# Kernel optimization log

Measured on AMD Instinct MI355X. Metric: run time of the kernel, lower is better.

## Reference

```python
import jax, jax.numpy as jnp
import numpy as np

B, N, IN_DIM, HEADS, PER_HEAD = 8, 512, 256, 4, 32
OUT_DIM = HEADS * PER_HEAD  # 128
NEG_SLOPE = 0.2


def setup_inputs() -> dict:
    key = jax.random.key(0)
    ks = jax.random.split(key, 8)
    x = jax.random.normal(ks[0], (B, N, IN_DIM), jnp.float32)
    adj = jax.random.randint(ks[1], (B, N, N), 0, 2, jnp.int32)
    sl = 1.0 / np.sqrt(IN_DIM)
    W_l = jax.random.normal(ks[2], (IN_DIM, OUT_DIM), jnp.float32) * sl  # source proj
    b_l = jnp.zeros((OUT_DIM,), jnp.float32)
    W_r = jax.random.normal(ks[3], (IN_DIM, OUT_DIM), jnp.float32) * sl  # target proj
    b_r = jnp.zeros((OUT_DIM,), jnp.float32)
    att = jax.random.normal(ks[4], (HEADS, PER_HEAD), jnp.float32) * (1.0 / np.sqrt(PER_HEAD))
    bias = jnp.zeros((OUT_DIM,), jnp.float32)
    return {"x": x, "adj": adj, "W_l": W_l, "b_l": b_l, "W_r": W_r, "b_r": b_r,
            "att": att, "bias": bias}


def _gatv2_single(x_b, adj_b, W_l, b_l, W_r, b_r, att, bias):
    # PyG GATv2Conv: remove_self_loops + add_self_loops -> diagonal forced to 1
    n = x_b.shape[0]
    adj_sl = jnp.fill_diagonal(adj_b, 1, inplace=False)
    # edge_index = adj.nonzero().t(): source = row, target = col
    m = (adj_sl != 0).T  # m[i, j]: source j feeds target i
    xl = (x_b @ W_l + b_l).reshape(n, HEADS, PER_HEAD)  # source-side features
    xr = (x_b @ W_r + b_r).reshape(n, HEADS, PER_HEAD)  # target-side features
    s = xr[:, None] + xl[None, :]                       # [i, j, H, C]
    s = jnp.where(s > 0, s, NEG_SLOPE * s)              # LeakyReLU(0.2)
    e = jnp.einsum('ijhc,hc->ijh', s, att)              # attention logits
    e = jnp.where(m[..., None], e, -jnp.inf)
    alpha = jax.nn.softmax(e, axis=1)                   # softmax over sources j
    out = jnp.einsum('ijh,jhc->ihc', alpha, xl).reshape(n, HEADS * PER_HEAD)
    return out + bias


def reference(x, adj, W_l, b_l, W_r, b_r, att, bias):
    # Sequential per-batch processing, faithful to the original Python loop
    # and keeping the [N,N,H,C] intermediate to one graph at a time.
    def one(args):
        x_b, adj_b = args
        return _gatv2_single(x_b, adj_b, W_l, b_l, W_r, b_r, att, bias)
    return jax.lax.map(one, (x, adj))  # [B, N, OUT_DIM]
```

## Files before the change

### kernel.cpp

```cpp
#include <hip/hip_runtime.h>
#include <hip/hip_bf16.h>

#define B_   8
#define N_   512
#define IND  256
#define H_   4
#define PH   32
#define OD   128
#define TI   4

typedef float v2f __attribute__((ext_vector_type(2)));

#define ATT_SCALE 0.5770780163555854f
#define DLR_SCALE 0.8656170245333781f

template <int PAT>
__device__ __forceinline__ float dpp_add(float x) {
    int yi = __builtin_amdgcn_mov_dpp(__float_as_int(x), PAT, 0xF, 0xF, true);
    return x + __int_as_float(yi);
}

__device__ __forceinline__ float fast_exp2(float x) {
#if __has_builtin(__builtin_amdgcn_exp2f)
    return __builtin_amdgcn_exp2f(x);
#else
    return exp2f(x);
#endif
}

__device__ __forceinline__ void pk_fma(v2f& d, v2f a, v2f b) {
    asm("v_pk_fma_f32 %0, %1, %2, %0" : "+v"(d) : "v"(a), "v"(b));
}

__global__ __launch_bounds__(256, 2) void proj_kernel(
    const float* __restrict__ x,
    const float* __restrict__ Wl, const float* __restrict__ bl,
    const float* __restrict__ Wr, const float* __restrict__ br,
    const float* __restrict__ att,
    float* __restrict__ xl, float* __restrict__ xr,
    float* __restrict__ dl, float* __restrict__ dr)
{
    __shared__ float xs[8 * IND];
    const int t = threadIdx.x;
    const int row0 = blockIdx.x * 8;

    const float4* xp4 = (const float4*)(x + (size_t)row0 * IND);
    float4* xs4 = (float4*)xs;
    #pragma unroll
    for (int k = 0; k < 2; ++k)
        xs4[t + k * 256] = xp4[t + k * 256];
    __syncthreads();

    const int which = t >> 7;
    const int rg = (t >> 6) & 1;
    const int og = t & 63;
    const int o0 = og * 2;
    const int r0 = rg * 4;
    const float* W  = which ? Wr : Wl;
    const float* bb = which ? br : bl;

    float acc0[4], acc1[4];
    #pragma unroll
    for (int r = 0; r < 4; ++r) { acc0[r] = 0.f; acc1[r] = 0.f; }

    for (int k = 0; k < IND; k += 4) {
        float wf0[4], wf1[4];
        #pragma unroll
        for (int kk = 0; kk < 4; ++kk) {
            float2 wv = *(const float2*)(W + (size_t)(k + kk) * OD + o0);
            wf0[kk] = wv.x;
            wf1[kk] = wv.y;
        }
        float xv[4][4];
        #pragma unroll
        for (int r = 0; r < 4; ++r)
            *(float4*)(xv[r]) = *(const float4*)(&xs[(r0 + r) * IND + k]);
        #pragma unroll
        for (int kk = 0; kk < 4; ++kk)
            #pragma unroll
            for (int r = 0; r < 4; ++r) {
                acc0[r] = fmaf(xv[r][kk], wf0[kk], acc0[r]);
                acc1[r] = fmaf(xv[r][kk], wf1[kk], acc1[r]);
            }
    }

    const float bv0 = bb[o0];
    const float bv1 = bb[o0 + 1];
    const float a0 = att[o0];
    const float a1 = att[o0 + 1];
    float* dst = which ? xr : xl;
    float* dp  = which ? dr : dl;
    float dcon[4];
    #pragma unroll
    for (int r = 0; r < 4; ++r) {
        float y0 = acc0[r] + bv0;
        float y1 = acc1[r] + bv1;
        *(float2*)(&dst[(size_t)(row0 + r0 + r) * OD + o0]) = make_float2(y0, y1);
        dcon[r] = fmaf(a0, y0, a1 * y1);
    }
    #pragma unroll
    for (int m = 1; m < 16; m <<= 1) {
        #pragma unroll
        for (int r = 0; r < 4; ++r)
            dcon[r] += __shfl_xor(dcon[r], m);
    }
    if ((og & 15) == 0) {
        const int h = og >> 4;
        #pragma unroll
        for (int r = 0; r < 4; ++r)
            dp[(size_t)(row0 + r0 + r) * H_ + h] = DLR_SCALE * dcon[r];
    }
}

__global__ __launch_bounds__(256, 3) void attn_kernel(
    const int* __restrict__ adj, const float* __restrict__ att,
    const float* __restrict__ bias,
    const float* __restrict__ xl, const float* __restrict__ xr,
    const float* __restrict__ dl, const float* __restrict__ dr,
    float* __restrict__ out)
{
    __shared__ float sacc[H_][16][TI][PH];
    __shared__ float ssum[H_][16][TI];

    const int t = threadIdx.x;
    const int b  = blockIdx.x >> 7;
    const int i0 = (blockIdx.x & 127) * TI;
    const int cq = t & 3;
    const int js = (t >> 2) & 15;
    const int h  = t >> 6;
    const int cbase = h * PH + cq * 8;

    float atS[8];
    {
        const float* ap = att + cbase;
        float4 a0 = *(const float4*)(ap);
        float4 a1 = *(const float4*)(ap + 4);
        atS[0] = ATT_SCALE * a0.x; atS[1] = ATT_SCALE * a0.y;
        atS[2] = ATT_SCALE * a0.z; atS[3] = ATT_SCALE * a0.w;
        atS[4] = ATT_SCALE * a1.x; atS[5] = ATT_SCALE * a1.y;
        atS[6] = ATT_SCALE * a1.z; atS[7] = ATT_SCALE * a1.w;
    }
    float xrS[TI][8];
    float drv[TI];
    #pragma unroll
    for (int il = 0; il < TI; ++il) {
        const float* xp = xr + ((size_t)(b * N_ + i0 + il)) * OD + cbase;
        float4 r0 = *(const float4*)(xp);
        float4 r1 = *(const float4*)(xp + 4);
        xrS[il][0] = r0.x; xrS[il][1] = r0.y; xrS[il][2] = r0.z; xrS[il][3] = r0.w;
        xrS[il][4] = r1.x; xrS[il][5] = r1.y; xrS[il][6] = r1.z; xrS[il][7] = r1.w;
        drv[il] = dr[((size_t)(b * N_ + i0 + il)) * H_ + h];
    }

    v2f acc[TI][4];
    float sumw[TI];
    #pragma unroll
    for (int il = 0; il < TI; ++il) {
        sumw[il] = 0.f;
        #pragma unroll
        for (int m = 0; m < 4; ++m) acc[il][m] = (v2f){0.f, 0.f};
    }

    const float* xlp = xl + ((size_t)(b * N_ + js)) * OD + cbase;
    const int*   ajp = adj + ((size_t)(b * N_ + js)) * N_ + i0;
    const float* dlp = dl + ((size_t)(b * N_ + js)) * H_ + h;

    float4 va = *(const float4*)(xlp);
    float4 vb = *(const float4*)(xlp + 4);
    int4   mj = *(const int4*)(ajp);
    float  dj = *dlp;

    #pragma unroll 2
    for (int u = 0; u < 32; ++u) {
        float4 wa = va, wb = vb;
        int4   wm = mj;
        float  wd = dj;
        if (u < 31) {
            xlp += 16 * OD; ajp += 16 * N_; dlp += 16 * H_;
            va = *(const float4*)(xlp);
            vb = *(const float4*)(xlp + 4);
            mj = *(const int4*)(ajp);
            dj = *dlp;
        }
        const int j = u * 16 + js;
        v2f p0 = (v2f){wa.x, wa.y}, p1 = (v2f){wa.z, wa.w};
        v2f p2 = (v2f){wb.x, wb.y}, p3 = (v2f){wb.z, wb.w};
        int wmv[4] = {wm.x, wm.y, wm.z, wm.w};
        #pragma unroll
        for (int il = 0; il < TI; ++il) {
            float s, e2a = 0.f, e2b = 0.f;
            s = xrS[il][0] + wa.x; e2a = fmaf(atS[0], __builtin_fabsf(s), e2a);
            s = xrS[il][1] + wa.y; e2b = fmaf(atS[1], __builtin_fabsf(s), e2b);
            s = xrS[il][2] + wa.z; e2a = fmaf(atS[2], __builtin_fabsf(s), e2a);
            s = xrS[il][3] + wa.w; e2b = fmaf(atS[3], __builtin_fabsf(s), e2b);
            s = xrS[il][4] + wb.x; e2a = fmaf(atS[4], __builtin_fabsf(s), e2a);
            s = xrS[il][5] + wb.y; e2b = fmaf(atS[5], __builtin_fabsf(s), e2b);
            s = xrS[il][6] + wb.z; e2a = fmaf(atS[6], __builtin_fabsf(s), e2a);
            s = xrS[il][7] + wb.w; e2b = fmaf(atS[7], __builtin_fabsf(s), e2b);
            float eh = e2a + e2b;
            eh = dpp_add<0xB1>(eh);
            eh = dpp_add<0x4E>(eh);
            float e = (wd + drv[il]) + eh;
            bool keep = (wmv[il] != 0) || (j == i0 + il);
            float w = keep ? fast_exp2(e) : 0.f;
            sumw[il] += w;
            v2f ws = (v2f){w, w};
            pk_fma(acc[il][0], ws, p0);
            pk_fma(acc[il][1], ws, p1);
            pk_fma(acc[il][2], ws, p2);
            pk_fma(acc[il][3], ws, p3);
        }
    }

    #pragma unroll
    for (int il = 0; il < TI; ++il) {
        float4 w0 = make_float4(acc[il][0].x, acc[il][0].y,
                                acc[il][1].x, acc[il][1].y);
        float4 w1 = make_float4(acc[il][2].x, acc[il][2].y,
                                acc[il][3].x, acc[il][3].y);
        *(float4*)(&sacc[h][js][il][cq * 8])     = w0;
        *(float4*)(&sacc[h][js][il][cq * 8 + 4]) = w1;
    }
    if (cq == 0) {
        #pragma unroll
        for (int il = 0; il < TI; ++il)
            ssum[h][js][il] = sumw[il];
    }
    __syncthreads();

    const int lane = t & 63;
    const int o = lane * 2;
    const int il2 = o >> 5;
    const int c2 = o & 31;
    float st = 0.f;
    #pragma unroll
    for (int k = 0; k < 16; ++k) st += ssum[h][k][il2];
    float a0 = 0.f, a1 = 0.f;
    #pragma unroll
    for (int k = 0; k < 16; ++k) {
        float2 p = *(const float2*)(&sacc[h][k][il2][c2]);
        a0 += p.x; a1 += p.y;
    }
    const float inv = 1.f / st;
    const int c = h * PH + c2;
    float* op = out + ((size_t)(b * N_ + i0 + il2)) * OD;
    *(float2*)(&op[c]) = make_float2(fmaf(a0, inv, bias[c]),
                                     fmaf(a1, inv, bias[c + 1]));
}

extern "C" void kernel_launch(void* const* d_in, const int* in_sizes, int n_in,
                              void* d_out, int out_size, void* d_ws, size_t ws_size,
                              hipStream_t stream) {
    const float* x    = (const float*)d_in[0];
    const int*   adj  = (const int*)d_in[1];
    const float* Wl   = (const float*)d_in[2];
    const float* bl   = (const float*)d_in[3];
    const float* Wr   = (const float*)d_in[4];
    const float* br   = (const float*)d_in[5];
    const float* att  = (const float*)d_in[6];
    const float* bias = (const float*)d_in[7];
    float* out = (float*)d_out;

    float* xl = (float*)d_ws;
    float* xr = xl + (size_t)B_ * N_ * OD;
    float* dl = xr + (size_t)B_ * N_ * OD;
    float* dr = dl + (size_t)B_ * N_ * H_;

    proj_kernel<<<512, 256, 0, stream>>>(x, Wl, bl, Wr, br, att, xl, xr, dl, dr);
    attn_kernel<<<1024, 256, 0, stream>>>(adj, att, bias, xl, xr, dl, dr, out);
}
```

Measured before the change: 122.0 us.

## Restructure attention to one target per block and split-K projection GEMM

The attention kernel now handles one target node per block. Each wave owns a head and each lane walks source nodes with stride 64, holding the full 32-channel head in registers, with the target's features made wave-uniform through readfirstlane. The grid grows from 1024 to 4096 blocks, and the XCD-aware block remapping is meant to spread batches across dies. The projection kernel switches to 4x4 register tiles with split-K over two half-waves, a software-prefetched K loop and a shared-memory combine. The aim is to cut cross-lane reductions and raise occupancy. In exchange, xl is re-read once per target instead of once per group of four targets, and adj is read with uncoalesced strided scalar loads.

```diff
diff --git a/kernel.cpp b/kernel.cpp
--- a/kernel.cpp
+++ b/kernel.cpp
@@ -1,5 +1,4 @@
 #include <hip/hip_runtime.h>
-#include <hip/hip_bf16.h>
 
 #define B_   8
 #define N_   512
@@ -7,17 +6,14 @@
 #define H_   4
 #define PH   32
 #define OD   128
-#define TI   4
 
 typedef float v2f __attribute__((ext_vector_type(2)));
 
 #define ATT_SCALE 0.5770780163555854f
 #define DLR_SCALE 0.8656170245333781f
 
-template <int PAT>
-__device__ __forceinline__ float dpp_add(float x) {
-    int yi = __builtin_amdgcn_mov_dpp(__float_as_int(x), PAT, 0xF, 0xF, true);
-    return x + __int_as_float(yi);
+__device__ __forceinline__ float rflf(float x) {
+    return __int_as_float(__builtin_amdgcn_readfirstlane(__float_as_int(x)));
 }
 
 __device__ __forceinline__ float fast_exp2(float x) {
@@ -41,211 +37,206 @@
     float* __restrict__ dl, float* __restrict__ dr)
 {
     __shared__ float xs[8 * IND];
+    __shared__ float comb[128][17];
+
     const int t = threadIdx.x;
     const int row0 = blockIdx.x * 8;
 
     const float4* xp4 = (const float4*)(x + (size_t)row0 * IND);
     float4* xs4 = (float4*)xs;
-    #pragma unroll
-    for (int k = 0; k < 2; ++k)
-        xs4[t + k * 256] = xp4[t + k * 256];
+    xs4[t]       = xp4[t];
+    xs4[t + 256] = xp4[t + 256];
     __syncthreads();
 
+    const int og    = t & 31;
+    const int rr    = (t >> 5) & 1;
+    const int ks    = (t >> 6) & 1;
     const int which = t >> 7;
-    const int rg = (t >> 6) & 1;
-    const int og = t & 63;
-    const int o0 = og * 2;
-    const int r0 = rg * 4;
-    const float* W  = which ? Wr : Wl;
-    const float* bb = which ? br : bl;
-
-    float acc0[4], acc1[4];
-    #pragma unroll
-    for (int r = 0; r < 4; ++r) { acc0[r] = 0.f; acc1[r] = 0.f; }
-
-    for (int k = 0; k < IND; k += 4) {
-        float wf0[4], wf1[4];
-        #pragma unroll
-        for (int kk = 0; kk < 4; ++kk) {
-            float2 wv = *(const float2*)(W + (size_t)(k + kk) * OD + o0);
-            wf0[kk] = wv.x;
-            wf1[kk] = wv.y;
-        }
-        float xv[4][4];
-        #pragma unroll
-        for (int r = 0; r < 4; ++r)
-            *(float4*)(xv[r]) = *(const float4*)(&xs[(r0 + r) * IND + k]);
+    const int o0 = og * 4;
+    const int r0 = rr * 4;
+    const int k0 = ks * 128;
+    const float* W = which ? Wr : Wl;
+
+    float acc[4][4];
+    #pragma unroll
+    for (int r = 0; r < 4; ++r)
+        #pragma unroll
+        for (int c = 0; c < 4; ++c) acc[r][c] = 0.f;
+
+    const float* wp = W + (size_t)k0 * OD + o0;
+
+    float wc[4][4], xc[4][4];
+    #pragma unroll
+    for (int kk = 0; kk < 4; ++kk)
+        *(float4*)wc[kk] = *(const float4*)(wp + (size_t)kk * OD);
+    #pragma unroll
+    for (int r = 0; r < 4; ++r)
+        *(float4*)xc[r] = *(const float4*)(&xs[(r0 + r) * IND + k0]);
+
+    #pragma unroll 4
+    for (int s = 0; s < 32; ++s) {
+        float wn[4][4], xn[4][4];
+        if (s < 31) {
+            const float* wq = wp + (size_t)(s + 1) * 4 * OD;
+            #pragma unroll
+            for (int kk = 0; kk < 4; ++kk)
+                *(float4*)wn[kk] = *(const float4*)(wq + (size_t)kk * OD);
+            const int kb = k0 + (s + 1) * 4;
+            #pragma unroll
+            for (int r = 0; r < 4; ++r)
+                *(float4*)xn[r] = *(const float4*)(&xs[(r0 + r) * IND + kb]);
+        }
         #pragma unroll
         for (int kk = 0; kk < 4; ++kk)
             #pragma unroll
-            for (int r = 0; r < 4; ++r) {
-                acc0[r] = fmaf(xv[r][kk], wf0[kk], acc0[r]);
-                acc1[r] = fmaf(xv[r][kk], wf1[kk], acc1[r]);
-            }
-    }
-
-    const float bv0 = bb[o0];
-    const float bv1 = bb[o0 + 1];
-    const float a0 = att[o0];
-    const float a1 = att[o0 + 1];
-    float* dst = which ? xr : xl;
-    float* dp  = which ? dr : dl;
-    float dcon[4];
-    #pragma unroll
-    for (int r = 0; r < 4; ++r) {
-        float y0 = acc0[r] + bv0;
-        float y1 = acc1[r] + bv1;
-        *(float2*)(&dst[(size_t)(row0 + r0 + r) * OD + o0]) = make_float2(y0, y1);
-        dcon[r] = fmaf(a0, y0, a1 * y1);
-    }
-    #pragma unroll
-    for (int m = 1; m < 16; m <<= 1) {
-        #pragma unroll
-        for (int r = 0; r < 4; ++r)
-            dcon[r] += __shfl_xor(dcon[r], m);
-    }
-    if ((og & 15) == 0) {
-        const int h = og >> 4;
-        #pragma unroll
-        for (int r = 0; r < 4; ++r)
-            dp[(size_t)(row0 + r0 + r) * H_ + h] = DLR_SCALE * dcon[r];
-    }
-}
-
-__global__ __launch_bounds__(256, 3) void attn_kernel(
+            for (int r = 0; r < 4; ++r)
+                #pragma unroll
+                for (int c = 0; c < 4; ++c)
+                    acc[r][c] = fmaf(xc[r][kk], wc[kk][c], acc[r][c]);
+        #pragma unroll
+        for (int kk = 0; kk < 4; ++kk) *(float4*)wc[kk] = *(float4*)wn[kk];
+        #pragma unroll
+        for (int r = 0; r < 4; ++r)    *(float4*)xc[r]  = *(float4*)xn[r];
+    }
+
+    const int pid = (t & 63) | ((t & 128) >> 1);
+    if (ks == 1) {
+        #pragma unroll
+        for (int i = 0; i < 16; ++i) comb[pid][i] = acc[i >> 2][i & 3];
+    }
+    __syncthreads();
+    if (ks == 0) {
+        const float* bb  = which ? br : bl;
+        float* dst = which ? xr : xl;
+        float* dp  = which ? dr : dl;
+        float4 bv = *(const float4*)(bb + o0);
+        float4 av = *(const float4*)(att + o0);
+        const float bvf[4] = {bv.x, bv.y, bv.z, bv.w};
+        const float avf[4] = {av.x, av.y, av.z, av.w};
+        #pragma unroll
+        for (int r = 0; r < 4; ++r) {
+            float y[4];
+            #pragma unroll
+            for (int c = 0; c < 4; ++c)
+                y[c] = (acc[r][c] + comb[pid][r * 4 + c]) + bvf[c];
+            *(float4*)(&dst[(size_t)(row0 + r0 + r) * OD + o0]) =
+                make_float4(y[0], y[1], y[2], y[3]);
+            float dc = fmaf(avf[0], y[0], fmaf(avf[1], y[1],
+                       fmaf(avf[2], y[2], avf[3] * y[3])));
+            dc += __shfl_xor(dc, 1);
+            dc += __shfl_xor(dc, 2);
+            dc += __shfl_xor(dc, 4);
+            if ((og & 7) == 0)
+                dp[(size_t)(row0 + r0 + r) * H_ + (og >> 3)] = DLR_SCALE * dc;
+        }
+    }
+}
+
+__global__ __launch_bounds__(256, 4) void attn_kernel(
     const int* __restrict__ adj, const float* __restrict__ att,
     const float* __restrict__ bias,
     const float* __restrict__ xl, const float* __restrict__ xr,
     const float* __restrict__ dl, const float* __restrict__ dr,
     float* __restrict__ out)
 {
-    __shared__ float sacc[H_][16][TI][PH];
-    __shared__ float ssum[H_][16][TI];
+    __shared__ float sacc[H_][64][PH + 1];
 
     const int t = threadIdx.x;
-    const int b  = blockIdx.x >> 7;
-    const int i0 = (blockIdx.x & 127) * TI;
-    const int cq = t & 3;
-    const int js = (t >> 2) & 15;
-    const int h  = t >> 6;
-    const int cbase = h * PH + cq * 8;
-
-    float atS[8];
+    const int bid = (blockIdx.x & 7) * (B_ * N_ / 8) + (blockIdx.x >> 3);
+    const int b    = bid >> 9;
+    const int i0   = bid & (N_ - 1);
+    const int lane = t & 63;
+    const int h    = __builtin_amdgcn_readfirstlane(t >> 6);
+    const int cbase = h * PH;
+
+    float xrS[PH], atS[PH];
     {
+        const float* xp = xr + ((size_t)(b * N_ + i0)) * OD + cbase;
         const float* ap = att + cbase;
-        float4 a0 = *(const float4*)(ap);
-        float4 a1 = *(const float4*)(ap + 4);
-        atS[0] = ATT_SCALE * a0.x; atS[1] = ATT_SCALE * a0.y;
-        atS[2] = ATT_SCALE * a0.z; atS[3] = ATT_SCALE * a0.w;
-        atS[4] = ATT_SCALE * a1.x; atS[5] = ATT_SCALE * a1.y;
-        atS[6] = ATT_SCALE * a1.z; atS[7] = ATT_SCALE * a1.w;
-    }
-    float xrS[TI][8];
-    float drv[TI];
-    #pragma unroll
-    for (int il = 0; il < TI; ++il) {
-        const float* xp = xr + ((size_t)(b * N_ + i0 + il)) * OD + cbase;
-        float4 r0 = *(const float4*)(xp);
-        float4 r1 = *(const float4*)(xp + 4);
-        xrS[il][0] = r0.x; xrS[il][1] = r0.y; xrS[il][2] = r0.z; xrS[il][3] = r0.w;
-        xrS[il][4] = r1.x; xrS[il][5] = r1.y; xrS[il][6] = r1.z; xrS[il][7] = r1.w;
-        drv[il] = dr[((size_t)(b * N_ + i0 + il)) * H_ + h];
-    }
-
-    v2f acc[TI][4];
-    float sumw[TI];
-    #pragma unroll
-    for (int il = 0; il < TI; ++il) {
-        sumw[il] = 0.f;
-        #pragma unroll
-        for (int m = 0; m < 4; ++m) acc[il][m] = (v2f){0.f, 0.f};
-    }
-
-    const float* xlp = xl + ((size_t)(b * N_ + js)) * OD + cbase;
-    const int*   ajp = adj + ((size_t)(b * N_ + js)) * N_ + i0;
-    const float* dlp = dl + ((size_t)(b * N_ + js)) * H_ + h;
-
-    float4 va = *(const float4*)(xlp);
-    float4 vb = *(const float4*)(xlp + 4);
-    int4   mj = *(const int4*)(ajp);
-    float  dj = *dlp;
-
-    #pragma unroll 2
-    for (int u = 0; u < 32; ++u) {
-        float4 wa = va, wb = vb;
-        int4   wm = mj;
-        float  wd = dj;
-        if (u < 31) {
-            xlp += 16 * OD; ajp += 16 * N_; dlp += 16 * H_;
-            va = *(const float4*)(xlp);
-            vb = *(const float4*)(xlp + 4);
-            mj = *(const int4*)(ajp);
-            dj = *dlp;
-        }
-        const int j = u * 16 + js;
-        v2f p0 = (v2f){wa.x, wa.y}, p1 = (v2f){wa.z, wa.w};
-        v2f p2 = (v2f){wb.x, wb.y}, p3 = (v2f){wb.z, wb.w};
-        int wmv[4] = {wm.x, wm.y, wm.z, wm.w};
-        #pragma unroll
-        for (int il = 0; il < TI; ++il) {
-            float s, e2a = 0.f, e2b = 0.f;
-            s = xrS[il][0] + wa.x; e2a = fmaf(atS[0], __builtin_fabsf(s), e2a);
-            s = xrS[il][1] + wa.y; e2b = fmaf(atS[1], __builtin_fabsf(s), e2b);
-            s = xrS[il][2] + wa.z; e2a = fmaf(atS[2], __builtin_fabsf(s), e2a);
-            s = xrS[il][3] + wa.w; e2b = fmaf(atS[3], __builtin_fabsf(s), e2b);
-            s = xrS[il][4] + wb.x; e2a = fmaf(atS[4], __builtin_fabsf(s), e2a);
-            s = xrS[il][5] + wb.y; e2b = fmaf(atS[5], __builtin_fabsf(s), e2b);
-            s = xrS[il][6] + wb.z; e2a = fmaf(atS[6], __builtin_fabsf(s), e2a);
-            s = xrS[il][7] + wb.w; e2b = fmaf(atS[7], __builtin_fabsf(s), e2b);
-            float eh = e2a + e2b;
-            eh = dpp_add<0xB1>(eh);
-            eh = dpp_add<0x4E>(eh);
-            float e = (wd + drv[il]) + eh;
-            bool keep = (wmv[il] != 0) || (j == i0 + il);
-            float w = keep ? fast_exp2(e) : 0.f;
-            sumw[il] += w;
-            v2f ws = (v2f){w, w};
-            pk_fma(acc[il][0], ws, p0);
-            pk_fma(acc[il][1], ws, p1);
-            pk_fma(acc[il][2], ws, p2);
-            pk_fma(acc[il][3], ws, p3);
-        }
-    }
-
-    #pragma unroll
-    for (int il = 0; il < TI; ++il) {
-        float4 w0 = make_float4(acc[il][0].x, acc[il][0].y,
-                                acc[il][1].x, acc[il][1].y);
-        float4 w1 = make_float4(acc[il][2].x, acc[il][2].y,
-                                acc[il][3].x, acc[il][3].y);
-        *(float4*)(&sacc[h][js][il][cq * 8])     = w0;
-        *(float4*)(&sacc[h][js][il][cq * 8 + 4]) = w1;
-    }
-    if (cq == 0) {
-        #pragma unroll
-        for (int il = 0; il < TI; ++il)
-            ssum[h][js][il] = sumw[il];
+        #pragma unroll
+        for (int q = 0; q < 8; ++q) {
+            float4 v = *(const float4*)(xp + q * 4);
+            float4 a = *(const float4*)(ap + q * 4);
+            xrS[q * 4 + 0] = rflf(v.x); xrS[q * 4 + 1] = rflf(v.y);
+            xrS[q * 4 + 2] = rflf(v.z); xrS[q * 4 + 3] = rflf(v.w);
+            atS[q * 4 + 0] = rflf(ATT_SCALE * a.x);
+            atS[q * 4 + 1] = rflf(ATT_SCALE * a.y);
+            atS[q * 4 + 2] = rflf(ATT_SCALE * a.z);
+            atS[q * 4 + 3] = rflf(ATT_SCALE * a.w);
+        }
+    }
+    const float drS = rflf(dr[((size_t)(b * N_ + i0)) * H_ + h]);
+
+    v2f acc[16];
+    #pragma unroll
+    for (int m = 0; m < 16; ++m) acc[m] = (v2f){0.f, 0.f};
+    float sumw = 0.f;
+
+    const float* xlp = xl + ((size_t)(b * N_ + lane)) * OD + cbase;
+    const int*   ajp = adj + ((size_t)(b * N_ + lane)) * N_ + i0;
+    const float* dlp = dl + ((size_t)(b * N_ + lane)) * H_ + h;
+
+    #pragma unroll
+    for (int u = 0; u < 8; ++u) {
+        float4 xq[8];
+        #pragma unroll
+        for (int q = 0; q < 8; ++q)
+            xq[q] = *(const float4*)(xlp + (size_t)u * 64 * OD + q * 4);
+        const int   aj = ajp[(size_t)u * 64 * N_];
+        const float wd = dlp[(size_t)u * 64 * H_];
+
+        float e0 = 0.f, e1 = 0.f, e2 = 0.f, e3 = 0.f;
+        #pragma unroll
+        for (int q = 0; q < 8; ++q) {
+            float s0 = xrS[q * 4 + 0] + xq[q].x;
+            float s1 = xrS[q * 4 + 1] + xq[q].y;
+            float s2 = xrS[q * 4 + 2] + xq[q].z;
+            float s3 = xrS[q * 4 + 3] + xq[q].w;
+            e0 = fmaf(atS[q * 4 + 0], __builtin_fabsf(s0), e0);
+            e1 = fmaf(atS[q * 4 + 1], __builtin_fabsf(s1), e1);
+            e2 = fmaf(atS[q * 4 + 2], __builtin_fabsf(s2), e2);
+            e3 = fmaf(atS[q * 4 + 3], __builtin_fabsf(s3), e3);
+        }
+        float e = ((wd + drS) + (e0 + e1)) + (e2 + e3);
+        const int j = u * 64 + lane;
+        bool keep = (aj != 0) || (j == i0);
+        float w = keep ? fast_exp2(e) : 0.f;
+        sumw += w;
+        v2f ws = (v2f){w, w};
+        #pragma unroll
+        for (int q = 0; q < 8; ++q) {
+            pk_fma(acc[q * 2 + 0], ws, (v2f){xq[q].x, xq[q].y});
+            pk_fma(acc[q * 2 + 1], ws, (v2f){xq[q].z, xq[q].w});
+        }
+    }
+
+    #pragma unroll
+    for (int m = 1; m < 64; m <<= 1) sumw += __shfl_xor(sumw, m);
+    const float inv = 1.f / sumw;
+
+    #pragma unroll
+    for (int m = 0; m < 16; ++m) {
+        sacc[h][lane][2 * m]     = acc[m].x;
+        sacc[h][lane][2 * m + 1] = acc[m].y;
     }
     __syncthreads();
 
-    const int lane = t & 63;
-    const int o = lane * 2;
-    const int il2 = o >> 5;
-    const int c2 = o & 31;
-    float st = 0.f;
-    #pragma unroll
-    for (int k = 0; k < 16; ++k) st += ssum[h][k][il2];
-    float a0 = 0.f, a1 = 0.f;
-    #pragma unroll
-    for (int k = 0; k < 16; ++k) {
-        float2 p = *(const float2*)(&sacc[h][k][il2][c2]);
-        a0 += p.x; a1 += p.y;
-    }
-    const float inv = 1.f / st;
-    const int c = h * PH + c2;
-    float* op = out + ((size_t)(b * N_ + i0 + il2)) * OD;
-    *(float2*)(&op[c]) = make_float2(fmaf(a0, inv, bias[c]),
-                                     fmaf(a1, inv, bias[c + 1]));
+    const int c  = lane & 31;
+    const int hf = lane >> 5;
+    float s0 = 0.f, s1 = 0.f, s2 = 0.f, s3 = 0.f;
+    #pragma unroll
+    for (int k = 0; k < 32; k += 4) {
+        s0 += sacc[h][hf * 32 + k + 0][c];
+        s1 += sacc[h][hf * 32 + k + 1][c];
+        s2 += sacc[h][hf * 32 + k + 2][c];
+        s3 += sacc[h][hf * 32 + k + 3][c];
+    }
+    float s = (s0 + s1) + (s2 + s3);
+    s += __shfl_xor(s, 32);
+    if (hf == 0) {
+        const int cg = cbase + c;
+        out[((size_t)(b * N_ + i0)) * OD + cg] = fmaf(s, inv, bias[cg]);
+    }
 }
 
 extern "C" void kernel_launch(void* const* d_in, const int* in_sizes, int n_in,
@@ -267,5 +258,5 @@
     float* dr = dl + (size_t)B_ * N_ * H_;
 
     proj_kernel<<<512, 256, 0, stream>>>(x, Wl, bl, Wr, br, att, xl, xr, dl, dr);
-    attn_kernel<<<1024, 256, 0, stream>>>(adj, att, bias, xl, xr, dl, dr, out);
-}
+    attn_kernel<<<4096, 256, 0, stream>>>(adj, att, bias, xl, xr, dl, dr, out);
+}
```

Result: slower. 279.9 us (+129.5%).
